# Performance work log

Measured on AMD Instinct MI355X. Metric: run time of the kernel, lower is better.

The kernel has to match this reference:

```python
import jax, jax.numpy as jnp
import numpy as np

# TDNN with context [-2, 2], full_context=True -> kernel_width 5.
# The original per-timestep index_select + tiny conv1d loop is, for full context,
# exactly a single VALID 1D convolution over time, followed by ReLU.

B, T, D_IN, D_OUT, KW = 32, 1024, 512, 512, 5


def setup_inputs() -> dict:
    key = jax.random.key(0)
    k1, k2, k3 = jax.random.split(key, 3)
    stdv = 1.0 / np.sqrt(D_IN)
    x = jax.random.normal(k1, (B, T, D_IN), dtype=jnp.float32)
    kernel = jax.random.normal(k2, (D_OUT, D_IN, KW), dtype=jnp.float32) * stdv
    bias = jax.random.normal(k3, (D_OUT,), dtype=jnp.float32) * stdv
    return {"x": x, "kernel": kernel, "bias": bias}


def reference(x, kernel, bias):
    # x: [B, T, D_in] -> [B, D_in, T] to match torch conv1d layout
    xc = jnp.transpose(x, (0, 2, 1))
    # VALID conv over time; kernel layout OIW matches torch (out, in, width)
    out = jax.lax.conv_general_dilated(
        xc, kernel,
        window_strides=(1,),
        padding="VALID",
        dimension_numbers=("NCW", "OIW", "NCW"),
    )  # [B, D_out, T - KW + 1]
    out = out + bias[None, :, None]
    return jax.nn.relu(out)
```

## Files before the change

kernel.cpp:

```cpp
#include <hip/hip_runtime.h>
#include <stdint.h>

#define BATCH 32
#define TLEN  1024
#define DIN   512
#define DOUT  512
#define KW    5
#define TOUT  1020
#define KDIM  (DIN * KW)

#define BM 128
#define BN 128
#define BK 32

typedef __attribute__((ext_vector_type(8))) short bf16x8;
typedef __attribute__((ext_vector_type(4))) float f32x4;

__device__ __forceinline__ uint16_t f2bf(float f) {
    uint32_t u = __float_as_uint(f);
    uint32_t r = u + 0x7FFFu + ((u >> 16) & 1u);
    return (uint16_t)(r >> 16);
}

__global__ void convert_x(const float4* __restrict__ x, uint4* __restrict__ xb) {
    int idx = blockIdx.x * blockDim.x + threadIdx.x;
    float4 a = x[2 * idx];
    float4 b = x[2 * idx + 1];
    uint4 v;
    v.x = (uint32_t)f2bf(a.x) | ((uint32_t)f2bf(a.y) << 16);
    v.y = (uint32_t)f2bf(a.z) | ((uint32_t)f2bf(a.w) << 16);
    v.z = (uint32_t)f2bf(b.x) | ((uint32_t)f2bf(b.y) << 16);
    v.w = (uint32_t)f2bf(b.z) | ((uint32_t)f2bf(b.w) << 16);
    xb[idx] = v;
}

__global__ void pack_w(const float* __restrict__ w, uint16_t* __restrict__ wb) {
    int idx = blockIdx.x * blockDim.x + threadIdx.x;
    int o   = idx / KDIM;
    int rem = idx - o * KDIM;
    int k   = rem >> 9;
    int i   = rem & 511;
    wb[idx] = f2bf(w[(o * DIN + i) * KW + k]);
}

__global__ void tdnn_gemm(const uint16_t* __restrict__ xb,
                          const uint16_t* __restrict__ wb,
                          const float* __restrict__ bias,
                          float* __restrict__ out) {
    __shared__ uint16_t As[BM * BK];
    __shared__ uint16_t Bs[BN * BK];

    const int tile = blockIdx.x;
    const int nb   = tile & 3;
    const int tb   = (tile >> 2) & 7;
    const int b    = tile >> 5;
    const int t0   = tb * BM;
    const int n0   = nb * BN;

    const int tid  = threadIdx.x;
    const int lane = tid & 63;
    const int w    = tid >> 6;
    const int m_wave = (w & 1) * 64;
    const int n_wave = (w >> 1) * 64;

    const uint16_t* xrow = xb + (size_t)b * TLEN * DIN + (size_t)t0 * DIN;

    f32x4 acc[4][4] = {};

    const int ml = lane & 15;
    const int kq = (lane >> 4) * 8;

    for (int kb = 0; kb < KDIM; kb += BK) {
        #pragma unroll
        for (int i = 0; i < 2; ++i) {
            int c   = w * 128 + i * 64 + lane;
            int row = c >> 2;
            int cc  = c & 3;
            const uint16_t* gp = xrow + row * DIN + kb + cc * 8;
            const uint16_t* lp = &As[(w * 128 + i * 64) * 8];
            __builtin_amdgcn_global_load_lds(
                (const __attribute__((address_space(1))) void*)gp,
                (__attribute__((address_space(3))) void*)lp, 16, 0, 0);
        }
        #pragma unroll
        for (int i = 0; i < 2; ++i) {
            int c   = w * 128 + i * 64 + lane;
            int row = c >> 2;
            int cc  = c & 3;
            const uint16_t* gp = wb + (size_t)(n0 + row) * KDIM + kb + cc * 8;
            const uint16_t* lp = &Bs[(w * 128 + i * 64) * 8];
            __builtin_amdgcn_global_load_lds(
                (const __attribute__((address_space(1))) void*)gp,
                (__attribute__((address_space(3))) void*)lp, 16, 0, 0);
        }
        __syncthreads();

        bf16x8 af[4], bfr[4];
        #pragma unroll
        for (int mi = 0; mi < 4; ++mi)
            af[mi] = *(const bf16x8*)&As[(m_wave + mi * 16 + ml) * BK + kq];
        #pragma unroll
        for (int ni = 0; ni < 4; ++ni)
            bfr[ni] = *(const bf16x8*)&Bs[(n_wave + ni * 16 + ml) * BK + kq];

        #pragma unroll
        for (int mi = 0; mi < 4; ++mi)
            #pragma unroll
            for (int ni = 0; ni < 4; ++ni)
                acc[mi][ni] = __builtin_amdgcn_mfma_f32_16x16x32_bf16(
                    af[mi], bfr[ni], acc[mi][ni], 0, 0, 0);
        __syncthreads();
    }

    const int rq = (lane >> 4) * 4;
    #pragma unroll
    for (int ni = 0; ni < 4; ++ni) {
        int o = n0 + n_wave + ni * 16 + ml;
        float bv = bias[o];
        float* orow = out + ((size_t)b * DOUT + o) * TOUT;
        #pragma unroll
        for (int mi = 0; mi < 4; ++mi) {
            int tbase = t0 + m_wave + mi * 16 + rq;
            #pragma unroll
            for (int r = 0; r < 4; ++r) {
                int t = tbase + r;
                if (t < TOUT) {
                    float v = acc[mi][ni][r] + bv;
                    orow[t] = v > 0.0f ? v : 0.0f;
                }
            }
        }
    }
}

extern "C" void kernel_launch(void* const* d_in, const int* in_sizes, int n_in,
                              void* d_out, int out_size, void* d_ws, size_t ws_size,
                              hipStream_t stream) {
    const float* x    = (const float*)d_in[0];
    const float* wgt  = (const float*)d_in[1];
    const float* bias = (const float*)d_in[2];
    float* out = (float*)d_out;

    uint16_t* xb = (uint16_t*)d_ws;
    uint16_t* wb = (uint16_t*)((char*)d_ws + (size_t)BATCH * TLEN * DIN * 2);

    convert_x<<<8192, 256, 0, stream>>>((const float4*)x, (uint4*)xb);
    pack_w<<<5120, 256, 0, stream>>>(wgt, wb);
    tdnn_gemm<<<1024, 256, 0, stream>>>(xb, wb, bias, out);
}
```

Before: 240.1 us.

## Double K-tile, XOR-swizzle LDS, remap blocks per XCD, fuse prep kernels

```diff
diff --git a/kernel.cpp b/kernel.cpp
--- a/kernel.cpp
+++ b/kernel.cpp
@@ -11,7 +11,7 @@
 
 #define BM 128
 #define BN 128
-#define BK 32
+#define BK 64
 
 typedef __attribute__((ext_vector_type(8))) short bf16x8;
 typedef __attribute__((ext_vector_type(4))) float f32x4;
@@ -22,38 +22,44 @@
     return (uint16_t)(r >> 16);
 }
 
-__global__ void convert_x(const float4* __restrict__ x, uint4* __restrict__ xb) {
-    int idx = blockIdx.x * blockDim.x + threadIdx.x;
-    float4 a = x[2 * idx];
-    float4 b = x[2 * idx + 1];
-    uint4 v;
-    v.x = (uint32_t)f2bf(a.x) | ((uint32_t)f2bf(a.y) << 16);
-    v.y = (uint32_t)f2bf(a.z) | ((uint32_t)f2bf(a.w) << 16);
-    v.z = (uint32_t)f2bf(b.x) | ((uint32_t)f2bf(b.y) << 16);
-    v.w = (uint32_t)f2bf(b.z) | ((uint32_t)f2bf(b.w) << 16);
-    xb[idx] = v;
+__global__ void convert_pack(const float4* __restrict__ x, uint4* __restrict__ xb,
+                             const float* __restrict__ w, uint16_t* __restrict__ wb) {
+    int bid = blockIdx.x;
+    if (bid < 8192) {
+        int idx = bid * 256 + threadIdx.x;
+        float4 a = x[2 * idx];
+        float4 b = x[2 * idx + 1];
+        uint4 v;
+        v.x = (uint32_t)f2bf(a.x) | ((uint32_t)f2bf(a.y) << 16);
+        v.y = (uint32_t)f2bf(a.z) | ((uint32_t)f2bf(a.w) << 16);
+        v.z = (uint32_t)f2bf(b.x) | ((uint32_t)f2bf(b.y) << 16);
+        v.w = (uint32_t)f2bf(b.z) | ((uint32_t)f2bf(b.w) << 16);
+        xb[idx] = v;
+    } else {
+        int idx = (bid - 8192) * 256 + threadIdx.x;
+        int o   = idx / KDIM;
+        int rem = idx - o * KDIM;
+        int k   = rem >> 9;
+        int i   = rem & 511;
+        wb[idx] = f2bf(w[(o * DIN + i) * KW + k]);
+    }
 }
 
-__global__ void pack_w(const float* __restrict__ w, uint16_t* __restrict__ wb) {
-    int idx = blockIdx.x * blockDim.x + threadIdx.x;
-    int o   = idx / KDIM;
-    int rem = idx - o * KDIM;
-    int k   = rem >> 9;
-    int i   = rem & 511;
-    wb[idx] = f2bf(w[(o * DIN + i) * KW + k]);
-}
-
-__global__ void tdnn_gemm(const uint16_t* __restrict__ xb,
-                          const uint16_t* __restrict__ wb,
-                          const float* __restrict__ bias,
-                          float* __restrict__ out) {
+__global__ void __launch_bounds__(256, 4)
+tdnn_gemm(const uint16_t* __restrict__ xb,
+          const uint16_t* __restrict__ wb,
+          const float* __restrict__ bias,
+          float* __restrict__ out) {
     __shared__ uint16_t As[BM * BK];
     __shared__ uint16_t Bs[BN * BK];
 
-    const int tile = blockIdx.x;
-    const int nb   = tile & 3;
-    const int tb   = (tile >> 2) & 7;
-    const int b    = tile >> 5;
+    const int j    = blockIdx.x;
+    const int xcd  = j & 7;
+    const int nb   = (j >> 3) & 3;
+    const int gi   = j >> 5;
+    const int g    = gi * 8 + xcd;
+    const int b    = g >> 3;
+    const int tb   = g & 7;
     const int t0   = tb * BM;
     const int n0   = nb * BN;
 
@@ -64,51 +70,61 @@
     const int n_wave = (w >> 1) * 64;
 
     const uint16_t* xrow = xb + (size_t)b * TLEN * DIN + (size_t)t0 * DIN;
+    const uint16_t* wrow = wb + (size_t)n0 * KDIM;
 
     f32x4 acc[4][4] = {};
 
     const int ml = lane & 15;
-    const int kq = (lane >> 4) * 8;
+    const int kg = lane >> 4;
 
     for (int kb = 0; kb < KDIM; kb += BK) {
         #pragma unroll
-        for (int i = 0; i < 2; ++i) {
-            int c   = w * 128 + i * 64 + lane;
-            int row = c >> 2;
-            int cc  = c & 3;
-            const uint16_t* gp = xrow + row * DIN + kb + cc * 8;
-            const uint16_t* lp = &As[(w * 128 + i * 64) * 8];
+        for (int i = 0; i < 4; ++i) {
+            int c    = w * 256 + i * 64 + lane;
+            int row  = c >> 3;
+            int slot = c & 7;
+            int ccg  = slot ^ (row & 7);
+            const uint16_t* gp = xrow + row * DIN + kb + ccg * 8;
+            const uint16_t* lp = &As[(w * 256 + i * 64) * 8];
             __builtin_amdgcn_global_load_lds(
                 (const __attribute__((address_space(1))) void*)gp,
                 (__attribute__((address_space(3))) void*)lp, 16, 0, 0);
         }
         #pragma unroll
-        for (int i = 0; i < 2; ++i) {
-            int c   = w * 128 + i * 64 + lane;
-            int row = c >> 2;
-            int cc  = c & 3;
-            const uint16_t* gp = wb + (size_t)(n0 + row) * KDIM + kb + cc * 8;
-            const uint16_t* lp = &Bs[(w * 128 + i * 64) * 8];
+        for (int i = 0; i < 4; ++i) {
+            int c    = w * 256 + i * 64 + lane;
+            int row  = c >> 3;
+            int slot = c & 7;
+            int ccg  = slot ^ (row & 7);
+            const uint16_t* gp = wrow + (size_t)row * KDIM + kb + ccg * 8;
+            const uint16_t* lp = &Bs[(w * 256 + i * 64) * 8];
             __builtin_amdgcn_global_load_lds(
                 (const __attribute__((address_space(1))) void*)gp,
                 (__attribute__((address_space(3))) void*)lp, 16, 0, 0);
         }
         __syncthreads();
 
-        bf16x8 af[4], bfr[4];
         #pragma unroll
-        for (int mi = 0; mi < 4; ++mi)
-            af[mi] = *(const bf16x8*)&As[(m_wave + mi * 16 + ml) * BK + kq];
-        #pragma unroll
-        for (int ni = 0; ni < 4; ++ni)
-            bfr[ni] = *(const bf16x8*)&Bs[(n_wave + ni * 16 + ml) * BK + kq];
-
-        #pragma unroll
-        for (int mi = 0; mi < 4; ++mi)
+        for (int h = 0; h < 2; ++h) {
+            const int cc = h * 4 + kg;
+            bf16x8 af[4], bfr[4];
             #pragma unroll
-            for (int ni = 0; ni < 4; ++ni)
-                acc[mi][ni] = __builtin_amdgcn_mfma_f32_16x16x32_bf16(
-                    af[mi], bfr[ni], acc[mi][ni], 0, 0, 0);
+            for (int mi = 0; mi < 4; ++mi) {
+                int r = m_wave + mi * 16 + ml;
+                af[mi] = *(const bf16x8*)&As[r * BK + (cc ^ (r & 7)) * 8];
+            }
+            #pragma unroll
+            for (int ni = 0; ni < 4; ++ni) {
+                int r = n_wave + ni * 16 + ml;
+                bfr[ni] = *(const bf16x8*)&Bs[r * BK + (cc ^ (r & 7)) * 8];
+            }
+            #pragma unroll
+            for (int mi = 0; mi < 4; ++mi)
+                #pragma unroll
+                for (int ni = 0; ni < 4; ++ni)
+                    acc[mi][ni] = __builtin_amdgcn_mfma_f32_16x16x32_bf16(
+                        af[mi], bfr[ni], acc[mi][ni], 0, 0, 0);
+        }
         __syncthreads();
     }
 
@@ -144,7 +160,6 @@
     uint16_t* xb = (uint16_t*)d_ws;
     uint16_t* wb = (uint16_t*)((char*)d_ws + (size_t)BATCH * TLEN * DIN * 2);
 
-    convert_x<<<8192, 256, 0, stream>>>((const float4*)x, (uint4*)xb);
-    pack_w<<<5120, 256, 0, stream>>>(wgt, wb);
+    convert_pack<<<13312, 256, 0, stream>>>((const float4*)x, (uint4*)xb, wgt, wb);
     tdnn_gemm<<<1024, 256, 0, stream>>>(xb, wb, bias, out);
 }
```

New measurement: 203.0 us. 15.4% less time.
